# Optimization experiments

Hardware: AMD Instinct MI355X
Metric: run time of the kernel (lower is better)

Reference implementation:

```python
import jax, jax.numpy as jnp
import numpy as np

EPS = 1e-5
HEADS, DK, DV, STRIDE, R = 8, 32, 32, 2, 4


def _conv(x, w, b, stride, pad, groups):
    y = jax.lax.conv_general_dilated(
        x, w, (stride, stride), [(pad, pad), (pad, pad)],
        dimension_numbers=('NCHW', 'OIHW', 'NCHW'),
        feature_group_count=groups)
    return y + b[None, :, None, None]


def _ln_chw(x):
    # torch F.layer_norm(x, [c, h, w]) with no affine: normalize over C,H,W per sample
    m = jnp.mean(x, axis=(1, 2, 3), keepdims=True)
    v = jnp.var(x, axis=(1, 2, 3), keepdims=True)
    return (x - m) * jax.lax.rsqrt(v + EPS)


def _bn(x, g, b, m, v):
    # eval-mode BatchNorm2d with running stats
    inv = jax.lax.rsqrt(v + EPS)
    return (x - m[None, :, None, None]) * (g * inv)[None, :, None, None] + b[None, :, None, None]


def _gelu(x):
    return jax.nn.gelu(x, approximate=False)  # torch nn.GELU default = exact erf


def _forward(x, lpu_w, lpu_b, dw_w, dw_b, wq, bq, wk, bk, wv, bv, wo, bo, pos_b,
             c1_w, c1_b, bn1_g, bn1_b, bn1_m, bn1_v,
             dw2_w, dw2_b, bn2_g, bn2_b, bn2_m, bn2_v,
             c2_w, c2_b, bn3_g, bn3_b, bn3_m, bn3_v):
    c = x.shape[1]
    # ---- LPU: depthwise 3x3 + residual ----
    x = _conv(x, lpu_w, lpu_b, 1, 1, c) + x
    b_, c, h, w = x.shape
    n = h * w
    # ---- LMHSA ----
    xn = _ln_chw(x)
    xr = xn.reshape(b_, c, n).transpose(0, 2, 1)                 # [b, N, c]
    q = (xr @ wq.T + bq).reshape(b_, n, HEADS, DK).transpose(0, 2, 1, 3)  # [b,H,N,dk]
    kv = _conv(x, dw_w, dw_b, STRIDE, 0, c)                      # note: on x (pre-LN), as in source
    nk = kv.shape[2] * kv.shape[3]
    kvr = kv.reshape(b_, c, nk).transpose(0, 2, 1)               # [b, Nk, c]
    k = (kvr @ wk.T + bk).reshape(b_, nk, HEADS, DK).transpose(0, 2, 1, 3)
    v = (kvr @ wv.T + bv).reshape(b_, nk, HEADS, DV).transpose(0, 2, 1, 3)
    att = jnp.einsum('bhid,bhjd->bhij', q, k) * (DK ** -0.5) + pos_b
    att = jax.nn.softmax(att, axis=-1)
    tmp = jnp.einsum('bhij,bhjd->bhid', att, v).transpose(0, 2, 1, 3).reshape(b_, n, HEADS * DV)
    # source does .view(b, d, h, w) on a contiguous [b, N, d] tensor -> raw row-major reinterpret
    x = (tmp @ wo.T + bo).reshape(b_, c, h, w) + x
    # ---- IRFFN ----
    t = _ln_chw(x)
    t = _gelu(_bn(_conv(t, c1_w, c1_b, 1, 0, 1), bn1_g, bn1_b, bn1_m, bn1_v))
    t = _gelu(_bn(_conv(t, dw2_w, dw2_b, 1, 1, t.shape[1]), bn2_g, bn2_b, bn2_m, bn2_v))
    t = _bn(_conv(t, c2_w, c2_b, 1, 0, 1), bn3_g, bn3_b, bn3_m, bn3_v)
    return x + t


def setup_inputs() -> dict:
    key = jax.random.key(0)
    ks = jax.random.split(key, 20)
    B_, C, H, W = 32, 256, 28, 28
    Cm = C * R
    N = H * W
    Nk = (H // STRIDE) * (W // STRIDE)
    r = lambda i, shape, s=0.02: jax.random.normal(ks[i], shape, jnp.float32) * s
    z = lambda n_: jnp.zeros((n_,), jnp.float32)
    o = lambda n_: jnp.ones((n_,), jnp.float32)
    return dict(
        x=jax.random.normal(ks[0], (B_, C, H, W), jnp.float32),
        lpu_w=r(1, (C, 1, 3, 3), 0.1), lpu_b=z(C),
        dw_w=r(2, (C, 1, STRIDE, STRIDE), 0.1), dw_b=z(C),
        wq=r(3, (HEADS * DK, C)), bq=z(HEADS * DK),
        wk=r(4, (HEADS * DK, C)), bk=z(HEADS * DK),
        wv=r(5, (HEADS * DV, C)), bv=z(HEADS * DV),
        wo=r(6, (C, HEADS * DK)), bo=z(C),
        pos_b=jax.random.normal(ks[7], (1, HEADS, N, Nk), jnp.float32),
        c1_w=r(8, (Cm, C, 1, 1)), c1_b=z(Cm),
        bn1_g=o(Cm), bn1_b=z(Cm), bn1_m=r(9, (Cm,), 0.1),
        bn1_v=jax.random.uniform(ks[10], (Cm,), jnp.float32, 0.5, 1.5),
        dw2_w=r(11, (Cm, 1, 3, 3), 0.1), dw2_b=z(Cm),
        bn2_g=o(Cm), bn2_b=z(Cm), bn2_m=r(12, (Cm,), 0.1),
        bn2_v=jax.random.uniform(ks[13], (Cm,), jnp.float32, 0.5, 1.5),
        c2_w=r(14, (C, Cm, 1, 1)), c2_b=z(C),
        bn3_g=o(C), bn3_b=z(C), bn3_m=r(15, (C,), 0.1),
        bn3_v=jax.random.uniform(ks[16], (C,), jnp.float32, 0.5, 1.5),
    )


def reference(x, lpu_w, lpu_b, dw_w, dw_b, wq, bq, wk, bk, wv, bv, wo, bo, pos_b,
              c1_w, c1_b, bn1_g, bn1_b, bn1_m, bn1_v,
              dw2_w, dw2_b, bn2_g, bn2_b, bn2_m, bn2_v,
              c2_w, c2_b, bn3_g, bn3_b, bn3_m, bn3_v):
    return _forward(x, lpu_w, lpu_b, dw_w, dw_b, wq, bq, wk, bk, wv, bv, wo, bo, pos_b,
                    c1_w, c1_b, bn1_g, bn1_b, bn1_m, bn1_v,
                    dw2_w, dw2_b, bn2_g, bn2_b, bn2_m, bn2_v,
                    c2_w, c2_b, bn3_g, bn3_b, bn3_m, bn3_v)
```

## Files before the change

### kernel.cpp

```cpp
#include <hip/hip_runtime.h>
#include <math.h>

#define B_ 32
#define C_ 256
#define H_ 28
#define W_ 28
#define NPIX 784
#define HK 14
#define NKPIX 196
#define CM 1024
#define EPS_ 1e-5f
#define LN_INVN (1.0f / (C_ * NPIX))

typedef __attribute__((ext_vector_type(8))) short short8;
typedef __attribute__((ext_vector_type(4))) short short4_;
typedef __attribute__((ext_vector_type(4))) float float4_;

__device__ __forceinline__ float gelu_f(float x) {
    return 0.5f * x * (1.0f + erff(x * 0.70710678118654752f));
}
__device__ __forceinline__ short f2bf(float f) {
    union { float f; unsigned u; } x; x.f = f;
    unsigned r = x.u + 0x7FFF + ((x.u >> 16) & 1);
    return (short)(r >> 16);
}
__device__ __forceinline__ float bf2f(short s) {
    union { unsigned u; float f; } x; x.u = ((unsigned)(unsigned short)s) << 16;
    return x.f;
}
__device__ __forceinline__ void gld16(const short* g, short* l) {
    __builtin_amdgcn_global_load_lds((const __attribute__((address_space(1))) void*)g,
                                     (__attribute__((address_space(3))) void*)l,
                                     16, 0, 0);
}

__global__ void wconv_kernel(const float* __restrict__ wq, const float* __restrict__ wk,
                             const float* __restrict__ wv, const float* __restrict__ wo,
                             const float* __restrict__ c1, const float* __restrict__ c2,
                             short* __restrict__ dst) {
    int idx = blockIdx.x * 256 + threadIdx.x;
    const float* src; int off;
    if (idx < 65536)       { src = wq; off = idx; }
    else if (idx < 131072) { src = wk; off = idx - 65536; }
    else if (idx < 196608) { src = wv; off = idx - 131072; }
    else if (idx < 262144) { src = wo; off = idx - 196608; }
    else if (idx < 524288) { src = c1; off = idx - 262144; }
    else                   { src = c2; off = idx - 524288; }
    dst[idx] = f2bf(src[off]);
}

__global__ void dwprep_kernel(const float* __restrict__ dww, const float* __restrict__ dwb,
                              const float* __restrict__ g2, const float* __restrict__ b2,
                              const float* __restrict__ m2, const float* __restrict__ v2,
                              float* __restrict__ wt, float* __restrict__ sc2,
                              float* __restrict__ sh2, float* __restrict__ st2) {
    int cm = blockIdx.x * 256 + threadIdx.x;
    if (blockIdx.x == 0 && threadIdx.x < 64) st2[threadIdx.x] = 0.f;
    float sc = g2[cm] * rsqrtf(v2[cm] + EPS_);
    sc2[cm] = sc;
    sh2[cm] = (dwb[cm] - m2[cm]) * sc + b2[cm];
    #pragma unroll
    for (int tap = 0; tap < 9; ++tap) wt[tap * 1024 + cm] = dww[cm * 9 + tap];
}

__global__ void lnreduce_kernel(const float* __restrict__ part, int cnt,
                                float* __restrict__ out) {
    int b = blockIdx.x;
    const float* p = part + (long)b * cnt * 2;
    float s = 0.f, s2 = 0.f;
    for (int i = threadIdx.x; i < cnt; i += 256) {
        s += p[i * 2];
        s2 += p[i * 2 + 1];
    }
    #pragma unroll
    for (int o = 32; o > 0; o >>= 1) {
        s += __shfl_down(s, o);
        s2 += __shfl_down(s2, o);
    }
    __shared__ float ss[4][2];
    int wv = threadIdx.x >> 6;
    if ((threadIdx.x & 63) == 0) { ss[wv][0] = s; ss[wv][1] = s2; }
    __syncthreads();
    if (threadIdx.x == 0) {
        out[b * 2]     = ss[0][0] + ss[1][0] + ss[2][0] + ss[3][0];
        out[b * 2 + 1] = ss[0][1] + ss[1][1] + ss[2][1] + ss[3][1];
    }
}

__global__ void lpu_kernel(const float* __restrict__ x, const float* __restrict__ w,
                           const float* __restrict__ bias, float* __restrict__ out,
                           float* __restrict__ part) {
    int idx4 = blockIdx.x * 256 + threadIdx.x;
    int chunk = idx4 % 196;
    int plane = idx4 / 196;
    int c = plane & 255;
    int p0 = chunk * 4;
    int py = p0 / W_, px0 = p0 % W_;
    const float* xp = x + (long)plane * NPIX;
    const float* wc = w + c * 9;
    float4 cc = *(const float4*)(xp + py * W_ + px0);
    float bb = bias[c];
    float acc0 = bb + cc.x, acc1 = bb + cc.y, acc2 = bb + cc.z, acc3 = bb + cc.w;
    #pragma unroll
    for (int dy = -1; dy <= 1; ++dy) {
        int yy = py + dy;
        if (yy < 0 || yy >= H_) continue;
        float4 v = (dy == 0) ? cc : *(const float4*)(xp + yy * W_ + px0);
        float vm1 = (px0 > 0)  ? xp[yy * W_ + px0 - 1] : 0.f;
        float v4  = (px0 < 24) ? xp[yy * W_ + px0 + 4] : 0.f;
        float w0 = wc[(dy + 1) * 3], w1 = wc[(dy + 1) * 3 + 1], w2 = wc[(dy + 1) * 3 + 2];
        acc0 += w0 * vm1 + w1 * v.x + w2 * v.y;
        acc1 += w0 * v.x + w1 * v.y + w2 * v.z;
        acc2 += w0 * v.y + w1 * v.z + w2 * v.w;
        acc3 += w0 * v.z + w1 * v.w + w2 * v4;
    }
    *(float4*)(out + (long)plane * NPIX + p0) = make_float4(acc0, acc1, acc2, acc3);
    float s = acc0 + acc1 + acc2 + acc3;
    float s2 = acc0 * acc0 + acc1 * acc1 + acc2 * acc2 + acc3 * acc3;
    #pragma unroll
    for (int o = 32; o > 0; o >>= 1) {
        s += __shfl_down(s, o);
        s2 += __shfl_down(s2, o);
    }
    __shared__ float ss[4][2];
    int wv = threadIdx.x >> 6;
    if ((threadIdx.x & 63) == 0) { ss[wv][0] = s; ss[wv][1] = s2; }
    __syncthreads();
    if (threadIdx.x == 0) {
        part[blockIdx.x * 2]     = ss[0][0] + ss[1][0] + ss[2][0] + ss[3][0];
        part[blockIdx.x * 2 + 1] = ss[0][1] + ss[1][1] + ss[2][1] + ss[3][1];
    }
}

__global__ void tln_kernel(const float* __restrict__ X, const float* __restrict__ st,
                           short* __restrict__ Y) {
    __shared__ float tile[32][33];
    int p0 = blockIdx.x * 32, c0 = blockIdx.y * 32, b = blockIdx.z;
    int tr = threadIdx.x >> 5, tc = threadIdx.x & 31;
    #pragma unroll
    for (int r = 0; r < 4; ++r) {
        int c = c0 + tr + r * 8, p = p0 + tc;
        tile[tr + r * 8][tc] = (p < NPIX) ? X[((long)b * C_ + c) * NPIX + p] : 0.f;
    }
    float sm = st[b * 2] * LN_INVN;
    float lr = rsqrtf(st[b * 2 + 1] * LN_INVN - sm * sm + EPS_);
    __syncthreads();
    #pragma unroll
    for (int r = 0; r < 4; ++r) {
        int p = p0 + tr + r * 8, c = c0 + tc;
        if (p < NPIX) Y[((long)b * NPIX + p) * C_ + c] = f2bf((tile[tc][tr + r * 8] - sm) * lr);
    }
}

__global__ void kvconv_kernel(const float* __restrict__ x1, const float* __restrict__ w,
                              const float* __restrict__ bias, short* __restrict__ out) {
    int idx = blockIdx.x * 256 + threadIdx.x;
    if (idx >= B_ * NKPIX * C_) return;
    int c = idx & 255;
    int rest = idx >> 8;
    int p = rest % NKPIX;
    int b = rest / NKPIX;
    int yo = p / HK, xo = p % HK;
    const float* xb = x1 + ((long)b * C_ + c) * NPIX;
    const float* wc = w + c * 4;
    float a = bias[c]
            + wc[0] * xb[(2 * yo) * W_ + 2 * xo]     + wc[1] * xb[(2 * yo) * W_ + 2 * xo + 1]
            + wc[2] * xb[(2 * yo + 1) * W_ + 2 * xo] + wc[3] * xb[(2 * yo + 1) * W_ + 2 * xo + 1];
    out[idx] = f2bf(a);
}

template <int EPI>
__global__ __launch_bounds__(256) void mfma_gemm(
    const short* __restrict__ Act, const short* __restrict__ Wb,
    int M, int N, int K,
    const float* __restrict__ bias,
    const float* __restrict__ g, const float* __restrict__ bb,
    const float* __restrict__ mm, const float* __restrict__ vv,
    const float* __restrict__ res, float* __restrict__ opart,
    short* __restrict__ outh, float* __restrict__ outf) {
    __shared__ short As[2 * 128 * 32];
    __shared__ short Bs[2 * 128 * 32];
    __shared__ float red[16][3];
    const int t = threadIdx.x;
    const int m0 = blockIdx.x * 128;
    const int n0 = blockIdx.y * 128;
    const int w = t >> 6, lane = t & 63;
    const int wm = (w & 1) * 64, wn = (w >> 1) * 64;
    const int col = lane & 15, quad = lane >> 4;

    float4_ acc[4][4];
    #pragma unroll
    for (int i = 0; i < 4; ++i)
        #pragma unroll
        for (int j = 0; j < 4; ++j)
            acc[i][j] = (float4_){0.f, 0.f, 0.f, 0.f};

    const int l4 = lane >> 2;
    const int segsw = (lane & 3) ^ ((l4 ^ (l4 >> 2)) & 3);
    const short* gA = Act + (long)(m0 + w * 16 + l4) * K + segsw * 8;
    const short* gB = Wb  + (long)(n0 + w * 16 + l4) * K + segsw * 8;
    const long rs64 = (long)64 * K;
    const int woff = w * 512;

    const int nk = K >> 5;
    {
        short* dA = As + woff;
        short* dB = Bs + woff;
        gld16(gA, dA);
        gld16(gA + rs64, dA + 2048);
        gld16(gB, dB);
        gld16(gB + rs64, dB + 2048);
    }
    const int slotsw = (quad ^ ((col & 3) ^ ((col >> 2) & 3))) * 8;

    for (int kt = 0; kt < nk; ++kt) {
        __syncthreads();
        const int cur = (kt & 1) * 4096;
        if (kt + 1 < nk) {
            const int nxtoff = ((kt + 1) & 1) * 4096 + woff;
            const int k0 = (kt + 1) * 32;
            gld16(gA + k0, As + nxtoff);
            gld16(gA + rs64 + k0, As + nxtoff + 2048);
            gld16(gB + k0, Bs + nxtoff);
            gld16(gB + rs64 + k0, Bs + nxtoff + 2048);
        }
        short8 af[4], bf[4];
        #pragma unroll
        for (int i = 0; i < 4; ++i)
            af[i] = *(const short8*)(As + cur + (wm + i * 16 + col) * 32 + slotsw);
        #pragma unroll
        for (int j = 0; j < 4; ++j)
            bf[j] = *(const short8*)(Bs + cur + (wn + j * 16 + col) * 32 + slotsw);
        #pragma unroll
        for (int i = 0; i < 4; ++i)
            #pragma unroll
            for (int j = 0; j < 4; ++j)
                acc[i][j] = __builtin_amdgcn_mfma_f32_16x16x32_bf16(af[i], bf[j], acc[i][j], 0, 0, 0);
    }

    #pragma unroll
    for (int i = 0; i < 4; ++i) {
        const int pbase = m0 + wm + i * 16 + quad * 4;
        float s1 = 0.f, s2s = 0.f;
        int bsmp = 0, psmp = 0;
        if (EPI == 3) { bsmp = pbase / NPIX; psmp = pbase - bsmp * NPIX; }
        #pragma unroll
        for (int j = 0; j < 4; ++j) {
            const int oc = n0 + wn + j * 16 + col;
            if (EPI == 0) {
                float cb = bias[oc];
                #pragma unroll
                for (int r = 0; r < 4; ++r)
                    outh[(long)(pbase + r) * N + oc] = f2bf(acc[i][j][r] + cb);
            } else if (EPI == 1) {
                float sc = g[oc] * rsqrtf(vv[oc] + EPS_);
                float sh = bb[oc] - mm[oc] * sc;
                float cb = bias[oc];
                #pragma unroll
                for (int r = 0; r < 4; ++r)
                    outh[(long)(pbase + r) * N + oc] =
                        f2bf(gelu_f((acc[i][j][r] + cb) * sc + sh));
            } else if (EPI == 2) {
                float cb = bias[oc];
                #pragma unroll
                for (int r = 0; r < 4; ++r) {
                    long jj = (long)(pbase + r) * 256 + oc;
                    float val = acc[i][j][r] + cb + res[jj];
                    outf[jj] = val;
                    s1 += val; s2s += val * val;
                }
            } else {
                float sc = g[oc] * rsqrtf(vv[oc] + EPS_);
                float sh = bb[oc] - mm[oc] * sc;
                float cb = bias[oc];
                long basei = ((long)bsmp * 256 + oc) * NPIX + psmp;
                float4 rv = *(const float4*)(res + basei);
                float4 y;
                y.x = (acc[i][j][0] + cb) * sc + sh + rv.x;
                y.y = (acc[i][j][1] + cb) * sc + sh + rv.y;
                y.z = (acc[i][j][2] + cb) * sc + sh + rv.z;
                y.w = (acc[i][j][3] + cb) * sc + sh + rv.w;
                *(float4*)(outf + basei) = y;
            }
        }
        if (EPI == 2) {
            #pragma unroll
            for (int o = 32; o > 0; o >>= 1) {
                s1 += __shfl_down(s1, o);
                s2s += __shfl_down(s2s, o);
            }
            if (lane == 0) {
                red[w * 4 + i][0] = (float)(pbase / NPIX);
                red[w * 4 + i][1] = s1;
                red[w * 4 + i][2] = s2s;
            }
        }
    }
    if (EPI == 2) {
        __syncthreads();
        if (t == 0) {
            int bsA = (int)red[0][0], bsB = -1;
            float a1 = 0.f, a2 = 0.f, b1 = 0.f, b2 = 0.f;
            #pragma unroll
            for (int e = 0; e < 16; ++e) {
                int bs = (int)red[e][0];
                if (bs == bsA) { a1 += red[e][1]; a2 += red[e][2]; }
                else           { bsB = bs; b1 += red[e][1]; b2 += red[e][2]; }
            }
            atomicAdd(&opart[bsA * 2], a1);
            atomicAdd(&opart[bsA * 2 + 1], a2);
            if (bsB >= 0) {
                atomicAdd(&opart[bsB * 2], b1);
                atomicAdd(&opart[bsB * 2 + 1], b2);
            }
        }
    }
}

__global__ __launch_bounds__(256) void attn_kernel(const short* __restrict__ q,
                                                   const short* __restrict__ k,
                                                   const short* __restrict__ v,
                                                   const float* __restrict__ pos_b,
                                                   short* __restrict__ out) {
    __shared__ short Ks[208 * 40];
    __shared__ short Vt[32 * 232];
    __shared__ float Ls[128];
    const int qt0 = blockIdx.x * 128;
    const int h = blockIdx.y;
    const int b = blockIdx.z;
    const int t = threadIdx.x;
    const short8 z8 = {0, 0, 0, 0, 0, 0, 0, 0};
    for (int e = t; e < 832; e += 256) {
        int row = e >> 2, seg = e & 3;
        short8 v8 = (row < NKPIX)
            ? *(const short8*)(k + ((long)(b * NKPIX + row)) * 256 + h * 32 + seg * 8) : z8;
        *(short8*)(Ks + row * 40 + seg * 8) = v8;
    }
    for (int e = t; e < 784; e += 256) {
        int key = e >> 2, seg = e & 3;
        short8 tv = *(const short8*)(v + ((long)(b * NKPIX + key)) * 256 + h * 32 + seg * 8);
        #pragma unroll
        for (int j = 0; j < 8; ++j) Vt[(seg * 8 + j) * 232 + key] = tv[j];
    }
    for (int e = t; e < 32 * 36; e += 256) {
        Vt[(e / 36) * 232 + 196 + (e % 36)] = 0;
    }
    __syncthreads();

    const int w = t >> 6, lane = t & 63;
    const int col = lane & 15, quad = lane >> 4;
    const float scale = 0.17677669529663689f;
    const float4_ z4 = {0.f, 0.f, 0.f, 0.f};

    short8 bq_[2];
    int qrow[2]; bool qvalid[2];
    const float* prow[2];
    #pragma unroll
    for (int i = 0; i < 2; ++i) {
        qrow[i] = qt0 + w * 32 + i * 16 + col;
        qvalid[i] = qrow[i] < NPIX;
        int qe = qvalid[i] ? qrow[i] : 0;
        bq_[i] = *(const short8*)(q + ((long)(b * NPIX + qe)) * 256 + h * 32 + quad * 8);
        prow[i] = pos_b + ((long)h * NPIX + qrow[i]) * NKPIX;
    }

    float4_ accO[2][2];
    #pragma unroll
    for (int i = 0; i < 2; ++i)
        #pragma unroll
        for (int nt = 0; nt < 2; ++nt) accO[i][nt] = z4;
    float lsum[2] = {0.f, 0.f};

    const int srcA = col + 32 * (quad & 1);
    const int srcB = srcA + 16;
    const bool hihalf = quad >= 2;

    #pragma unroll
    for (int kc = 0; kc < 4; ++kc) {
        const int base = kc * 64;
        const int ntn = (kc == 3) ? 1 : 4;
        unsigned long long v64[2][4];
        if (kc == 3) { v64[0][1] = 0ULL; v64[1][1] = 0ULL; }
        #pragma unroll
        for (int nt = 0; nt < 4; ++nt) {
            if (nt >= ntn) continue;
            short8 afk = *(const short8*)(Ks + (base + nt * 16 + col) * 40 + quad * 8);
            int keybase = base + nt * 16 + quad * 4;
            bool kval = keybase < NKPIX;
            #pragma unroll
            for (int i = 0; i < 2; ++i) {
                float4_ s4 = __builtin_amdgcn_mfma_f32_16x16x32_bf16(afk, bq_[i], z4, 0, 0, 0);
                float4 pv = make_float4(0.f, 0.f, 0.f, 0.f);
                bool valid = kval && qvalid[i];
                if (valid)
                    pv = *(const float4*)(prow[i] + keybase);
                float p0 = valid ? __expf(s4[0] * scale + pv.x) : 0.f;
                float p1 = valid ? __expf(s4[1] * scale + pv.y) : 0.f;
                float p2 = valid ? __expf(s4[2] * scale + pv.z) : 0.f;
                float p3 = valid ? __expf(s4[3] * scale + pv.w) : 0.f;
                lsum[i] += p0 + p1 + p2 + p3;
                unsigned lo = ((unsigned)(unsigned short)f2bf(p1) << 16) |
                              (unsigned)(unsigned short)f2bf(p0);
                unsigned hi = ((unsigned)(unsigned short)f2bf(p3) << 16) |
                              (unsigned)(unsigned short)f2bf(p2);
                v64[i][nt] = ((unsigned long long)hi << 32) | lo;
            }
        }
        const int ksn = (kc == 3) ? 1 : 2;
        #pragma unroll
        for (int ks = 0; ks < 2; ++ks) {
            if (ks >= ksn) continue;
            #pragma unroll
            for (int i = 0; i < 2; ++i) {
                unsigned long long sel = hihalf ? v64[i][2 * ks + 1] : v64[i][2 * ks];
                unsigned long long flo = __shfl(sel, srcA, 64);
                unsigned long long fhi = __shfl(sel, srcB, 64);
                union { unsigned long long u; short s[4]; } ul, uh;
                ul.u = flo; uh.u = fhi;
                short8 afp = { ul.s[0], ul.s[1], ul.s[2], ul.s[3],
                               uh.s[0], uh.s[1], uh.s[2], uh.s[3] };
                #pragma unroll
                for (int nt = 0; nt < 2; ++nt) {
                    short8 bfv = *(const short8*)(Vt + (nt * 16 + col) * 232 + base + ks * 32 + quad * 8);
                    accO[i][nt] = __builtin_amdgcn_mfma_f32_16x16x32_bf16(afp, bfv, accO[i][nt], 0, 0, 0);
                }
            }
        }
    }
    #pragma unroll
    for (int i = 0; i < 2; ++i) {
        float s = lsum[i];
        s += __shfl_xor(s, 16);
        s += __shfl_xor(s, 32);
        if (quad == 0) Ls[w * 32 + i * 16 + col] = 1.f / s;
    }
    __builtin_amdgcn_s_waitcnt(0);
    #pragma unroll
    for (int i = 0; i < 2; ++i) {
        int qb0 = qt0 + w * 32 + i * 16 + quad * 4;
        #pragma unroll
        for (int r = 0; r < 4; ++r) {
            int qq = qb0 + r;
            if (qq >= NPIX) continue;
            float rinv = Ls[w * 32 + i * 16 + quad * 4 + r];
            #pragma unroll
            for (int nt = 0; nt < 2; ++nt)
                out[((long)(b * NPIX + qq)) * 256 + h * 32 + nt * 16 + col] =
                    f2bf(accO[i][nt][r] * rinv);
        }
    }
}

__global__ __launch_bounds__(256) void dwgelu_kernel(
    const short* __restrict__ t2, const float* __restrict__ wt,
    const float* __restrict__ sc2, const float* __restrict__ sh2,
    short* __restrict__ t3) {
    const int nchunk = 3136 / 8;
    int bid = blockIdx.x;
    int swz = (bid & 7) * nchunk + (bid >> 3);
    int idx = swz * 256 + threadIdx.x;
    int cm8 = idx & 127;
    int rest = idx >> 7;
    int grp = rest % 196;
    int b = rest / 196;
    int py0 = (grp / 28) * 4;
    int px = grp % 28;
    int cm0 = cm8 * 8;
    const short* tb = t2 + ((long)b * NPIX) * CM + cm0;

    float wv[9][8];
    #pragma unroll
    for (int tp = 0; tp < 9; ++tp) {
        float4 a = *(const float4*)(wt + tp * 1024 + cm0);
        float4 bq = *(const float4*)(wt + tp * 1024 + cm0 + 4);
        wv[tp][0] = a.x;  wv[tp][1] = a.y;  wv[tp][2] = a.z;  wv[tp][3] = a.w;
        wv[tp][4] = bq.x; wv[tp][5] = bq.y; wv[tp][6] = bq.z; wv[tp][7] = bq.w;
    }

    float acc[4][8];
    #pragma unroll
    for (int k = 0; k < 4; ++k)
        #pragma unroll
        for (int c = 0; c < 8; ++c) acc[k][c] = 0.f;

    #pragma unroll
    for (int ro = -1; ro <= 4; ++ro) {
        int rr = py0 + ro;
        if (rr < 0 || rr >= H_) continue;
        const short* rowb = tb + (long)(rr * W_ + px) * CM;
        float fm[8], fc[8], fp[8];
        if (px > 0) {
            short8 s = *(const short8*)(rowb - CM);
            #pragma unroll
            for (int c = 0; c < 8; ++c) fm[c] = bf2f(s[c]);
        } else {
            #pragma unroll
            for (int c = 0; c < 8; ++c) fm[c] = 0.f;
        }
        {
            short8 s = *(const short8*)(rowb);
            #pragma unroll
            for (int c = 0; c < 8; ++c) fc[c] = bf2f(s[c]);
        }
        if (px < 27) {
            short8 s = *(const short8*)(rowb + CM);
            #pragma unroll
            for (int c = 0; c < 8; ++c) fp[c] = bf2f(s[c]);
        } else {
            #pragma unroll
            for (int c = 0; c < 8; ++c) fp[c] = 0.f;
        }
        #pragma unroll
        for (int k = 0; k < 4; ++k) {
            const int tr = ro - k + 1;
            if (tr < 0 || tr > 2) continue;
            #pragma unroll
            for (int c = 0; c < 8; ++c)
                acc[k][c] = fmaf(wv[tr * 3][c], fm[c],
                            fmaf(wv[tr * 3 + 1][c], fc[c],
                            fmaf(wv[tr * 3 + 2][c], fp[c], acc[k][c])));
        }
    }

    float4 sa = *(const float4*)(sc2 + cm0);
    float4 sb = *(const float4*)(sc2 + cm0 + 4);
    float4 ha = *(const float4*)(sh2 + cm0);
    float4 hb = *(const float4*)(sh2 + cm0 + 4);
    float scl[8] = {sa.x, sa.y, sa.z, sa.w, sb.x, sb.y, sb.z, sb.w};
    float shf[8] = {ha.x, ha.y, ha.z, ha.w, hb.x, hb.y, hb.z, hb.w};
    #pragma unroll
    for (int k = 0; k < 4; ++k) {
        short8 ov;
        #pragma unroll
        for (int c = 0; c < 8; ++c)
            ov[c] = f2bf(gelu_f(acc[k][c] * scl[c] + shf[c]));
        *(short8*)(t3 + ((long)b * NPIX + (py0 + k) * W_ + px) * CM + cm0) = ov;
    }
}

extern "C" void kernel_launch(void* const* d_in, const int* in_sizes, int n_in,
                              void* d_out, int out_size, void* d_ws, size_t ws_size,
                              hipStream_t stream) {
    const float* x     = (const float*)d_in[0];
    const float* lpu_w = (const float*)d_in[1];
    const float* lpu_b = (const float*)d_in[2];
    const float* dw_w  = (const float*)d_in[3];
    const float* dw_b  = (const float*)d_in[4];
    const float* wq    = (const float*)d_in[5];
    const float* bq    = (const float*)d_in[6];
    const float* wk    = (const float*)d_in[7];
    const float* bk    = (const float*)d_in[8];
    const float* wv    = (const float*)d_in[9];
    const float* bv    = (const float*)d_in[10];
    const float* wo    = (const float*)d_in[11];
    const float* bo    = (const float*)d_in[12];
    const float* posb  = (const float*)d_in[13];
    const float* c1_w  = (const float*)d_in[14];
    const float* c1_b  = (const float*)d_in[15];
    const float* bn1_g = (const float*)d_in[16];
    const float* bn1_b = (const float*)d_in[17];
    const float* bn1_m = (const float*)d_in[18];
    const float* bn1_v = (const float*)d_in[19];
    const float* dw2_w = (const float*)d_in[20];
    const float* dw2_b = (const float*)d_in[21];
    const float* bn2_g = (const float*)d_in[22];
    const float* bn2_b = (const float*)d_in[23];
    const float* bn2_m = (const float*)d_in[24];
    const float* bn2_v = (const float*)d_in[25];
    const float* c2_w  = (const float*)d_in[26];
    const float* c2_b  = (const float*)d_in[27];
    const float* bn3_g = (const float*)d_in[28];
    const float* bn3_b = (const float*)d_in[29];
    const float* bn3_m = (const float*)d_in[30];
    const float* bn3_v = (const float*)d_in[31];

    const long n1  = (long)B_ * C_ * NPIX;
    const long nkv = (long)B_ * C_ * NKPIX;
    const long nm  = (long)B_ * CM * NPIX;
    const int  nblk1 = (int)(n1 / 1024);
    const int  MQ = B_ * NPIX;
    const int  MKV = B_ * NKPIX;

    char* base = (char*)d_ws;
    float* x1   = (float*)base; base += n1 * 4;
    float* x2c  = (float*)base; base += n1 * 4;
    short* x1n  = (short*)base; base += n1 * 2;
    short* qb   = (short*)base; base += n1 * 2;
    short* tmpb = (short*)base; base += n1 * 2;
    short* t1n  = (short*)base; base += n1 * 2;
    short* kvb  = (short*)base; base += nkv * 2;
    short* kb   = (short*)base; base += nkv * 2;
    short* vb   = (short*)base; base += nkv * 2;
    short* t2   = (short*)base; base += nm * 2;
    short* t3   = (short*)base; base += nm * 2;
    short* wbf  = (short*)base; base += 786432L * 2;
    float* stats = (float*)base; base += 128 * 4;
    float* dwt   = (float*)base; base += 9216 * 4;
    float* dsc   = (float*)base; base += 1024 * 4;
    float* dsh   = (float*)base; base += 1024 * 4;
    float* part1 = (float*)base; base += (long)nblk1 * 2 * 4;
    float* outp = (float*)d_out;

    wconv_kernel<<<3072, 256, 0, stream>>>(wq, wk, wv, wo, c1_w, c2_w, wbf);
    dwprep_kernel<<<4, 256, 0, stream>>>(dw2_w, dw2_b, bn2_g, bn2_b, bn2_m, bn2_v,
                                         dwt, dsc, dsh, stats + 64);
    lpu_kernel<<<nblk1, 256, 0, stream>>>(x, lpu_w, lpu_b, x1, part1);
    lnreduce_kernel<<<B_, 256, 0, stream>>>(part1, nblk1 / B_, stats);
    kvconv_kernel<<<(int)((nkv + 255) / 256), 256, 0, stream>>>(x1, dw_w, dw_b, kvb);
    tln_kernel<<<dim3(25, 8, B_), 256, 0, stream>>>(x1, stats, x1n);
    mfma_gemm<0><<<dim3(MQ / 128, 2), 256, 0, stream>>>(
        x1n, wbf, MQ, 256, 256, bq, nullptr, nullptr, nullptr, nullptr,
        nullptr, nullptr, qb, nullptr);
    mfma_gemm<0><<<dim3(MKV / 128, 2), 256, 0, stream>>>(
        kvb, wbf + 65536, MKV, 256, 256, bk, nullptr, nullptr, nullptr, nullptr,
        nullptr, nullptr, kb, nullptr);
    mfma_gemm<0><<<dim3(MKV / 128, 2), 256, 0, stream>>>(
        kvb, wbf + 131072, MKV, 256, 256, bv, nullptr, nullptr, nullptr, nullptr,
        nullptr, nullptr, vb, nullptr);
    attn_kernel<<<dim3(7, 8, B_), 256, 0, stream>>>(qb, kb, vb, posb, tmpb);
    mfma_gemm<2><<<dim3(MQ / 128, 2), 256, 0, stream>>>(
        tmpb, wbf + 196608, MQ, 256, 256, bo, nullptr, nullptr, nullptr, nullptr,
        x1, stats + 64, nullptr, x2c);
    tln_kernel<<<dim3(25, 8, B_), 256, 0, stream>>>(x2c, stats + 64, t1n);
    mfma_gemm<1><<<dim3(MQ / 128, 8), 256, 0, stream>>>(
        t1n, wbf + 262144, MQ, CM, 256, c1_b, bn1_g, bn1_b, bn1_m, bn1_v,
        nullptr, nullptr, t2, nullptr);
    dwgelu_kernel<<<3136, 256, 0, stream>>>(t2, dwt, dsc, dsh, t3);
    mfma_gemm<3><<<dim3(MQ / 128, 2), 256, 0, stream>>>(
        t3, wbf + 524288, MQ, 256, 1024, c2_b, bn3_g, bn3_b, bn3_m, bn3_v,
        x2c, nullptr, nullptr, outp);
}
```

Before: 410.9 us.

## Transpose MFMA operands for vectorized epilogue stores and fuse K/V projections

For the row-major epilogues, the MFMA operands are swapped so each lane holds four consecutive output channels. This lets bias, BN parameters, residuals and outputs be loaded and stored as float4/short4 vectors instead of scalar strided accesses. The separate K and V projection GEMMs are merged into one launch with N=512, a new epilogue routes columns to the k or v buffers, and this assumes vb directly follows kb in the workspace. The change cuts epilogue memory transactions and one kernel launch, but adds layout coupling between buffers.

```diff
diff --git a/kernel.cpp b/kernel.cpp
--- a/kernel.cpp
+++ b/kernel.cpp
@@ -11,6 +11,7 @@
 #define CM 1024
 #define EPS_ 1e-5f
 #define LN_INVN (1.0f / (C_ * NPIX))
+#define KVN ((long)B_ * NKPIX * C_)
 
 typedef __attribute__((ext_vector_type(8))) short short8;
 typedef __attribute__((ext_vector_type(4))) short short4_;
@@ -234,42 +235,22 @@
         #pragma unroll
         for (int i = 0; i < 4; ++i)
             #pragma unroll
-            for (int j = 0; j < 4; ++j)
-                acc[i][j] = __builtin_amdgcn_mfma_f32_16x16x32_bf16(af[i], bf[j], acc[i][j], 0, 0, 0);
-    }
-
-    #pragma unroll
-    for (int i = 0; i < 4; ++i) {
-        const int pbase = m0 + wm + i * 16 + quad * 4;
-        float s1 = 0.f, s2s = 0.f;
-        int bsmp = 0, psmp = 0;
-        if (EPI == 3) { bsmp = pbase / NPIX; psmp = pbase - bsmp * NPIX; }
-        #pragma unroll
-        for (int j = 0; j < 4; ++j) {
-            const int oc = n0 + wn + j * 16 + col;
-            if (EPI == 0) {
-                float cb = bias[oc];
-                #pragma unroll
-                for (int r = 0; r < 4; ++r)
-                    outh[(long)(pbase + r) * N + oc] = f2bf(acc[i][j][r] + cb);
-            } else if (EPI == 1) {
-                float sc = g[oc] * rsqrtf(vv[oc] + EPS_);
-                float sh = bb[oc] - mm[oc] * sc;
-                float cb = bias[oc];
-                #pragma unroll
-                for (int r = 0; r < 4; ++r)
-                    outh[(long)(pbase + r) * N + oc] =
-                        f2bf(gelu_f((acc[i][j][r] + cb) * sc + sh));
-            } else if (EPI == 2) {
-                float cb = bias[oc];
-                #pragma unroll
-                for (int r = 0; r < 4; ++r) {
-                    long jj = (long)(pbase + r) * 256 + oc;
-                    float val = acc[i][j][r] + cb + res[jj];
-                    outf[jj] = val;
-                    s1 += val; s2s += val * val;
-                }
-            } else {
+            for (int j = 0; j < 4; ++j) {
+                if (EPI == 3)
+                    acc[i][j] = __builtin_amdgcn_mfma_f32_16x16x32_bf16(af[i], bf[j], acc[i][j], 0, 0, 0);
+                else
+                    acc[i][j] = __builtin_amdgcn_mfma_f32_16x16x32_bf16(bf[j], af[i], acc[i][j], 0, 0, 0);
+            }
+    }
+
+    if (EPI == 3) {
+        #pragma unroll
+        for (int i = 0; i < 4; ++i) {
+            const int pbase = m0 + wm + i * 16 + quad * 4;
+            int bsmp = pbase / NPIX, psmp = pbase - bsmp * NPIX;
+            #pragma unroll
+            for (int j = 0; j < 4; ++j) {
+                const int oc = n0 + wn + j * 16 + col;
                 float sc = g[oc] * rsqrtf(vv[oc] + EPS_);
                 float sh = bb[oc] - mm[oc] * sc;
                 float cb = bias[oc];
@@ -283,16 +264,67 @@
                 *(float4*)(outf + basei) = y;
             }
         }
-        if (EPI == 2) {
-            #pragma unroll
-            for (int o = 32; o > 0; o >>= 1) {
-                s1 += __shfl_down(s1, o);
-                s2s += __shfl_down(s2s, o);
-            }
-            if (lane == 0) {
-                red[w * 4 + i][0] = (float)(pbase / NPIX);
-                red[w * 4 + i][1] = s1;
-                red[w * 4 + i][2] = s2s;
+    } else {
+        #pragma unroll
+        for (int i = 0; i < 4; ++i) {
+            const int prow = m0 + wm + i * 16 + col;
+            float s1 = 0.f, s2s = 0.f;
+            #pragma unroll
+            for (int j = 0; j < 4; ++j) {
+                const int oc0 = n0 + wn + j * 16 + quad * 4;
+                if (EPI == 0) {
+                    float4 cb = *(const float4*)(bias + oc0);
+                    short4_ ov = { f2bf(acc[i][j][0] + cb.x), f2bf(acc[i][j][1] + cb.y),
+                                   f2bf(acc[i][j][2] + cb.z), f2bf(acc[i][j][3] + cb.w) };
+                    *(short4_*)(outh + (long)prow * N + oc0) = ov;
+                } else if (EPI == 4) {
+                    const int side = n0 >= 256;
+                    const float* bp = side ? (g + (oc0 - 256)) : (bias + oc0);
+                    float4 cb = *(const float4*)bp;
+                    short4_ ov = { f2bf(acc[i][j][0] + cb.x), f2bf(acc[i][j][1] + cb.y),
+                                   f2bf(acc[i][j][2] + cb.z), f2bf(acc[i][j][3] + cb.w) };
+                    *(short4_*)(outh + (long)side * KVN + (long)prow * 256 + (oc0 & 255)) = ov;
+                } else if (EPI == 1) {
+                    float4 g4 = *(const float4*)(g + oc0);
+                    float4 v4 = *(const float4*)(vv + oc0);
+                    float4 b4 = *(const float4*)(bb + oc0);
+                    float4 m4 = *(const float4*)(mm + oc0);
+                    float4 cb = *(const float4*)(bias + oc0);
+                    float sc0 = g4.x * rsqrtf(v4.x + EPS_);
+                    float sc1 = g4.y * rsqrtf(v4.y + EPS_);
+                    float sc2 = g4.z * rsqrtf(v4.z + EPS_);
+                    float sc3 = g4.w * rsqrtf(v4.w + EPS_);
+                    short4_ ov;
+                    ov[0] = f2bf(gelu_f((acc[i][j][0] + cb.x) * sc0 + (b4.x - m4.x * sc0)));
+                    ov[1] = f2bf(gelu_f((acc[i][j][1] + cb.y) * sc1 + (b4.y - m4.y * sc1)));
+                    ov[2] = f2bf(gelu_f((acc[i][j][2] + cb.z) * sc2 + (b4.z - m4.z * sc2)));
+                    ov[3] = f2bf(gelu_f((acc[i][j][3] + cb.w) * sc3 + (b4.w - m4.w * sc3)));
+                    *(short4_*)(outh + (long)prow * N + oc0) = ov;
+                } else {
+                    float4 cb = *(const float4*)(bias + oc0);
+                    long jj = (long)prow * 256 + oc0;
+                    float4 rv = *(const float4*)(res + jj);
+                    float4 y;
+                    y.x = acc[i][j][0] + cb.x + rv.x;
+                    y.y = acc[i][j][1] + cb.y + rv.y;
+                    y.z = acc[i][j][2] + cb.z + rv.z;
+                    y.w = acc[i][j][3] + cb.w + rv.w;
+                    *(float4*)(outf + jj) = y;
+                    s1 += y.x + y.y + y.z + y.w;
+                    s2s += y.x * y.x + y.y * y.y + y.z * y.z + y.w * y.w;
+                }
+            }
+            if (EPI == 2) {
+                #pragma unroll
+                for (int o = 32; o > 0; o >>= 1) {
+                    s1 += __shfl_down(s1, o);
+                    s2s += __shfl_down(s2s, o);
+                }
+                if (lane == 0) {
+                    red[w * 4 + i][0] = (float)((m0 + wm + i * 16) / NPIX);
+                    red[w * 4 + i][1] = s1;
+                    red[w * 4 + i][2] = s2s;
+                }
             }
         }
     }
@@ -611,12 +643,9 @@
     mfma_gemm<0><<<dim3(MQ / 128, 2), 256, 0, stream>>>(
         x1n, wbf, MQ, 256, 256, bq, nullptr, nullptr, nullptr, nullptr,
         nullptr, nullptr, qb, nullptr);
-    mfma_gemm<0><<<dim3(MKV / 128, 2), 256, 0, stream>>>(
-        kvb, wbf + 65536, MKV, 256, 256, bk, nullptr, nullptr, nullptr, nullptr,
+    mfma_gemm<4><<<dim3(MKV / 128, 4), 256, 0, stream>>>(
+        kvb, wbf + 65536, MKV, 512, 256, bk, bv, nullptr, nullptr, nullptr,
         nullptr, nullptr, kb, nullptr);
-    mfma_gemm<0><<<dim3(MKV / 128, 2), 256, 0, stream>>>(
-        kvb, wbf + 131072, MKV, 256, 256, bv, nullptr, nullptr, nullptr, nullptr,
-        nullptr, nullptr, vb, nullptr);
     attn_kernel<<<dim3(7, 8, B_), 256, 0, stream>>>(qb, kb, vb, posb, tmpb);
     mfma_gemm<2><<<dim3(MQ / 128, 2), 256, 0, stream>>>(
         tmpb, wbf + 196608, MQ, 256, 256, bo, nullptr, nullptr, nullptr, nullptr,
```

Result: no change. 417.2 us (+1.5%).
